# Optimization experiments

Hardware: AMD Instinct MI355X
Metric: run time of the kernel (lower is better)

## Reference

```python
import jax, jax.numpy as jnp
import numpy as np

INPUT_SIZE = 1024
HIDDEN_SIZE = 1024
LN_EPS = 1e-5


def setup_inputs() -> dict:
    key = jax.random.key(0)
    ks = jax.random.split(key, 8)
    bs, n = 4, 2048
    # Xavier-uniform bound for square (in=out) linear layers
    bound = float(np.sqrt(6.0 / (INPUT_SIZE + HIDDEN_SIZE)))
    x = jax.random.normal(ks[0], (bs, n, INPUT_SIZE), dtype=jnp.float32)
    wq = jax.random.uniform(ks[1], (INPUT_SIZE, HIDDEN_SIZE), jnp.float32, -bound, bound)
    wk = jax.random.uniform(ks[2], (INPUT_SIZE, HIDDEN_SIZE), jnp.float32, -bound, bound)
    wv = jax.random.uniform(ks[3], (INPUT_SIZE, HIDDEN_SIZE), jnp.float32, -bound, bound)
    bq = jnp.zeros((HIDDEN_SIZE,), jnp.float32)
    bk = jnp.zeros((HIDDEN_SIZE,), jnp.float32)
    bv = jnp.zeros((HIDDEN_SIZE,), jnp.float32)
    ln_w = jnp.ones((INPUT_SIZE,), jnp.float32)
    ln_b = jnp.zeros((INPUT_SIZE,), jnp.float32)
    return {"x": x, "wq": wq, "bq": bq, "wk": wk, "bk": bk,
            "wv": wv, "bv": bv, "ln_w": ln_w, "ln_b": ln_b}


def _layernorm(x, w, b):
    mu = jnp.mean(x, axis=-1, keepdims=True)
    var = jnp.mean(jnp.square(x - mu), axis=-1, keepdims=True)
    return (x - mu) * jax.lax.rsqrt(var + LN_EPS) * w + b


def reference(x, wq, bq, wk, bk, wv, bv, ln_w, ln_b):
    # x: [b, n, d_in]
    xn = _layernorm(x, ln_w, ln_b)
    q = jnp.einsum('bnd,dh->bnh', xn, wq) + bq
    k = jnp.einsum('bnd,dh->bnh', xn, wk) + bk
    v = jnp.einsum('bnd,dh->bnh', xn, wv) + bv
    scale = 1.0 / np.sqrt(HIDDEN_SIZE)
    att = jnp.einsum('bqh,bkh->bqk', q, k) * scale  # [b, n, n]
    att = jax.nn.softmax(att, axis=-1)
    out = jnp.einsum('bqk,bkh->bqh', att, v)  # [b, n, h]
    return (att, out)
```

## Files before the change

### kernel.cpp

```cpp
#include <hip/hip_runtime.h>
#include <stdint.h>


typedef __attribute__((ext_vector_type(8))) short short8;
typedef __attribute__((ext_vector_type(4))) float floatx4;
typedef __attribute__((ext_vector_type(4))) uint16_t u16x4;

__device__ __forceinline__ uint16_t f2bf(float f) {
    union { float f; uint32_t u; } v; v.f = f;
    uint32_t r = v.u + 0x7fffu + ((v.u >> 16) & 1u);
    return (uint16_t)(r >> 16);
}

typedef const uint32_t __attribute__((address_space(1)))* gas1_t;
typedef uint32_t __attribute__((address_space(3)))* las3_t;
__device__ __forceinline__ void gload_lds16(const uint16_t* g, uint16_t* l) {
    __builtin_amdgcn_global_load_lds((gas1_t)g, (las3_t)l, 16, 0, 0);
}

#define BM 128
#define BN 128
#define BK2 64

template<int EPI>
__device__ __forceinline__ void gemm_bt_body(
    const uint16_t* __restrict__ A, const uint16_t* __restrict__ Bt, int K,
    float* __restrict__ Cf, uint16_t* __restrict__ Cb, int ldc,
    const float* __restrict__ bias, float alpha)
{
    __shared__ uint16_t lA[BM * BK2];
    __shared__ uint16_t lB[BN * BK2];

    const int t  = threadIdx.x;
    const int m0 = blockIdx.y * BM;
    const int n0 = blockIdx.x * BN;

    const int srow = t >> 3;
    const int sseg = (t & 7) ^ (srow & 7);
    const uint16_t* ga = A + (size_t)(m0 + srow) * K + sseg * 8;
    const uint16_t* gb = Bt + (size_t)(n0 + srow) * K + sseg * 8;
    uint16_t* la = &lA[t * 8];
    uint16_t* lb = &lB[t * 8];
    const size_t rstep = (size_t)32 * K;

    const int lane = t & 63;
    const int w    = t >> 6;
    const int quad = lane >> 4;
    const int lrow = lane & 15;
    const int wm   = (w & 1) * 64;
    const int wn   = (w >> 1) * 64;
    const int swz  = lrow & 7;

    floatx4 acc[4][4];
#pragma unroll
    for (int i = 0; i < 4; i++)
#pragma unroll
        for (int j = 0; j < 4; j++)
            acc[i][j] = floatx4{0.f, 0.f, 0.f, 0.f};

    for (int k0 = 0; k0 < K; k0 += BK2) {
        __syncthreads();
        gload_lds16(ga + k0,             la);
        gload_lds16(ga + rstep + k0,     la + 2048);
        gload_lds16(ga + 2 * rstep + k0, la + 4096);
        gload_lds16(ga + 3 * rstep + k0, la + 6144);
        gload_lds16(gb + k0,             lb);
        gload_lds16(gb + rstep + k0,     lb + 2048);
        gload_lds16(gb + 2 * rstep + k0, lb + 4096);
        gload_lds16(gb + 3 * rstep + k0, lb + 6144);
        __syncthreads();

#pragma unroll
        for (int ks = 0; ks < 2; ks++) {
            short8 af[4], bf[4];
#pragma unroll
            for (int mi = 0; mi < 4; mi++)
                af[mi] = *(const short8*)&lA[(wm + mi * 16 + lrow) * BK2 +
                                             (((ks * 4 + quad) ^ swz) * 8)];
#pragma unroll
            for (int ni = 0; ni < 4; ni++)
                bf[ni] = *(const short8*)&lB[(wn + ni * 16 + lrow) * BK2 +
                                             (((ks * 4 + quad) ^ swz) * 8)];
#pragma unroll
            for (int mi = 0; mi < 4; mi++)
#pragma unroll
                for (int ni = 0; ni < 4; ni++)
                    acc[mi][ni] = __builtin_amdgcn_mfma_f32_16x16x32_bf16(
                        af[mi], bf[ni], acc[mi][ni], 0, 0, 0);
        }
    }

#pragma unroll
    for (int mi = 0; mi < 4; mi++) {
#pragma unroll
        for (int ni = 0; ni < 4; ni++) {
            const int row = m0 + wm + mi * 16 + quad * 4;
            const int col = n0 + wn + ni * 16 + lrow;
#pragma unroll
            for (int r = 0; r < 4; r++) {
                const float v = acc[mi][ni][r];
                if (EPI == 0) {
                    Cf[(size_t)(row + r) * ldc + col] = v * alpha;
                } else if (EPI == 1) {
                    Cb[(size_t)(row + r) * ldc + col] = f2bf(v + bias[col]);
                } else {
                    Cf[(size_t)(row + r) * ldc + col] = v;
                }
            }
        }
    }
}

__global__ __launch_bounds__(256) void k_qkv(
    const uint16_t* __restrict__ xn, const uint16_t* __restrict__ wt,
    const float* __restrict__ bq, const float* __restrict__ bk,
    const float* __restrict__ bv, uint16_t* __restrict__ qkv)
{
    const int z = blockIdx.z;
    const uint16_t* Bt = wt + (size_t)z * 1024 * 1024;
    const float* bias = (z == 0) ? bq : ((z == 1) ? bk : bv);
    uint16_t* C = qkv + (size_t)z * 8192 * 1024;
    gemm_bt_body<1>(xn, Bt, 1024, nullptr, C, 1024, bias, 0.f);
}

__global__ __launch_bounds__(256) void k_scores(
    const uint16_t* __restrict__ q, const uint16_t* __restrict__ k,
    float* __restrict__ S)
{
    const int z = blockIdx.z;
    gemm_bt_body<0>(q + (size_t)z * 2048 * 1024, k + (size_t)z * 2048 * 1024, 1024,
                    S + (size_t)z * 2048 * 2048, nullptr, 2048, nullptr, 0.03125f);
}

__global__ __launch_bounds__(256) void k_out(
    const uint16_t* __restrict__ attb, const uint16_t* __restrict__ vt,
    float* __restrict__ out)
{
    const int z = blockIdx.z;
    gemm_bt_body<2>(attb + (size_t)z * 2048 * 2048, vt + (size_t)z * 1024 * 2048, 2048,
                    out + (size_t)z * 2048 * 1024, nullptr, 1024, nullptr, 0.f);
}

__global__ __launch_bounds__(256) void k_ln(
    const float* __restrict__ x, const float* __restrict__ lw,
    const float* __restrict__ lb, uint16_t* __restrict__ xn)
{
    const int row = blockIdx.x;
    const int t = threadIdx.x;
    const float* xr = x + (size_t)row * 1024;
    const float4 xv = ((const float4*)xr)[t];
    float s  = xv.x + xv.y + xv.z + xv.w;
    float s2 = xv.x * xv.x + xv.y * xv.y + xv.z * xv.z + xv.w * xv.w;
#pragma unroll
    for (int off = 32; off > 0; off >>= 1) {
        s  += __shfl_xor(s, off);
        s2 += __shfl_xor(s2, off);
    }
    __shared__ float ps[4], ps2[4];
    const int w = t >> 6, lane = t & 63;
    if (lane == 0) { ps[w] = s; ps2[w] = s2; }
    __syncthreads();
    s  = ps[0] + ps[1] + ps[2] + ps[3];
    s2 = ps2[0] + ps2[1] + ps2[2] + ps2[3];
    const float mu  = s * (1.f / 1024.f);
    const float var = s2 * (1.f / 1024.f) - mu * mu;
    const float rs  = rsqrtf(var + 1e-5f);
    const float4 wv = ((const float4*)lw)[t];
    const float4 bv = ((const float4*)lb)[t];
    u16x4 o;
    o.x = f2bf((xv.x - mu) * rs * wv.x + bv.x);
    o.y = f2bf((xv.y - mu) * rs * wv.y + bv.y);
    o.z = f2bf((xv.z - mu) * rs * wv.z + bv.z);
    o.w = f2bf((xv.w - mu) * rs * wv.w + bv.w);
    ((u16x4*)(xn + (size_t)row * 1024))[t] = o;
}

__global__ void k_wt(const float* __restrict__ wq, const float* __restrict__ wk,
                     const float* __restrict__ wv, uint16_t* __restrict__ wt)
{
    __shared__ float tile[32][33];
    const int z = blockIdx.z;
    const float* W = (z == 0) ? wq : ((z == 1) ? wk : wv);
    uint16_t* T = wt + (size_t)z * 1024 * 1024;
    const int c0 = blockIdx.x * 32, r0 = blockIdx.y * 32;
    const int tx = threadIdx.x, ty = threadIdx.y;
#pragma unroll
    for (int i = 0; i < 4; i++)
        tile[ty + 8 * i][tx] = W[(size_t)(r0 + ty + 8 * i) * 1024 + c0 + tx];
    __syncthreads();
#pragma unroll
    for (int i = 0; i < 4; i++)
        T[(size_t)(c0 + ty + 8 * i) * 1024 + r0 + tx] = f2bf(tile[tx][ty + 8 * i]);
}

__global__ __launch_bounds__(256) void k_vt(
    const uint16_t* __restrict__ v, uint16_t* __restrict__ vt)
{
    __shared__ uint16_t tile[64][68];
    const int b = blockIdx.z;
    const uint16_t* V = v + (size_t)b * 2048 * 1024;
    uint16_t* T = vt + (size_t)b * 1024 * 2048;
    const int h0 = blockIdx.x * 64, t0 = blockIdx.y * 64;
    const int t = threadIdx.x;
    const int rr = t >> 4;
    const int cc = (t & 15) * 4;
#pragma unroll
    for (int i = 0; i < 4; i++) {
        const int tok = rr + 16 * i;
        *(u16x4*)&tile[tok][cc] =
            *(const u16x4*)&V[(size_t)(t0 + tok) * 1024 + h0 + cc];
    }
    __syncthreads();
#pragma unroll
    for (int i = 0; i < 4; i++) {
        const int h = rr + 16 * i;
        u16x4 o;
        o.x = tile[cc + 0][h];
        o.y = tile[cc + 1][h];
        o.z = tile[cc + 2][h];
        o.w = tile[cc + 3][h];
        *(u16x4*)&T[(size_t)(h0 + h) * 2048 + t0 + cc] = o;
    }
}

__global__ __launch_bounds__(256) void k_softmax(
    float* __restrict__ S, uint16_t* __restrict__ attb)
{
    const size_t row = blockIdx.x;
    float* p = S + row * 2048;
    const int t = threadIdx.x;
    float4 a = ((float4*)p)[2 * t];
    float4 b = ((float4*)p)[2 * t + 1];
    float m = fmaxf(fmaxf(fmaxf(a.x, a.y), fmaxf(a.z, a.w)),
                    fmaxf(fmaxf(b.x, b.y), fmaxf(b.z, b.w)));
#pragma unroll
    for (int off = 32; off > 0; off >>= 1) m = fmaxf(m, __shfl_xor(m, off));
    __shared__ float pm[4], pl[4];
    const int w = t >> 6, lane = t & 63;
    if (lane == 0) pm[w] = m;
    __syncthreads();
    m = fmaxf(fmaxf(pm[0], pm[1]), fmaxf(pm[2], pm[3]));

    a.x = __expf(a.x - m); a.y = __expf(a.y - m);
    a.z = __expf(a.z - m); a.w = __expf(a.w - m);
    b.x = __expf(b.x - m); b.y = __expf(b.y - m);
    b.z = __expf(b.z - m); b.w = __expf(b.w - m);
    float s = a.x + a.y + a.z + a.w + b.x + b.y + b.z + b.w;
#pragma unroll
    for (int off = 32; off > 0; off >>= 1) s += __shfl_xor(s, off);
    if (lane == 0) pl[w] = s;
    __syncthreads();
    s = pl[0] + pl[1] + pl[2] + pl[3];
    const float inv = 1.f / s;

    a.x *= inv; a.y *= inv; a.z *= inv; a.w *= inv;
    b.x *= inv; b.y *= inv; b.z *= inv; b.w *= inv;
    ((float4*)p)[2 * t]     = a;
    ((float4*)p)[2 * t + 1] = b;

    uint16_t* q = attb + row * 2048 + t * 8;
    u16x4 o0, o1;
    o0.x = f2bf(a.x); o0.y = f2bf(a.y); o0.z = f2bf(a.z); o0.w = f2bf(a.w);
    o1.x = f2bf(b.x); o1.y = f2bf(b.y); o1.z = f2bf(b.z); o1.w = f2bf(b.w);
    ((u16x4*)q)[0] = o0;
    ((u16x4*)q)[1] = o1;
}

extern "C" void kernel_launch(void* const* d_in, const int* in_sizes, int n_in,
                              void* d_out, int out_size, void* d_ws, size_t ws_size,
                              hipStream_t stream)
{
    const float* x  = (const float*)d_in[0];
    const float* wq = (const float*)d_in[1];
    const float* bq = (const float*)d_in[2];
    const float* wk = (const float*)d_in[3];
    const float* bk = (const float*)d_in[4];
    const float* wv = (const float*)d_in[5];
    const float* bv = (const float*)d_in[6];
    const float* lw = (const float*)d_in[7];
    const float* lb = (const float*)d_in[8];

    float* att = (float*)d_out;
    float* out = (float*)d_out + (size_t)16777216;

    uint16_t* xn = (uint16_t*)d_out;
    uint16_t* wt = (uint16_t*)d_out + (size_t)8388608;

    uint16_t* ws   = (uint16_t*)d_ws;
    uint16_t* q    = ws;
    uint16_t* k    = ws + (size_t)8388608;
    uint16_t* v    = ws + (size_t)2 * 8388608;
    uint16_t* vt   = ws;
    uint16_t* attb = ws + (size_t)8388608;
    uint16_t* qkv  = q;

    if (ws_size < (size_t)50331648) return;

    k_ln<<<8192, 256, 0, stream>>>(x, lw, lb, xn);
    k_wt<<<dim3(32, 32, 3), dim3(32, 8), 0, stream>>>(wq, wk, wv, wt);
    k_qkv<<<dim3(8, 64, 3), 256, 0, stream>>>(xn, wt, bq, bk, bv, qkv);
    k_scores<<<dim3(16, 16, 4), 256, 0, stream>>>(q, k, att);
    k_vt<<<dim3(16, 32, 4), 256, 0, stream>>>(v, vt);
    k_softmax<<<8192, 256, 0, stream>>>(att, attb);
    k_out<<<dim3(8, 16, 4), 256, 0, stream>>>(attb, vt, out);
}
```

Baseline: 338.0 us.

## Double-buffer LDS tiles in bf16 GEMM with K-step prefetch

Cuts the GEMM K-tile from 64 to 32 and splits LDS into two buffers. The next tile's global-to-LDS loads are issued before the current tile's MFMA work, which leaves one barrier per iteration instead of two. The aim is to overlap memory latency with compute. In exchange each barrier covers half as much MFMA work, and the XOR swizzle shrinks to 4 segments, which may raise LDS bank conflicts.

```diff
diff --git a/kernel.cpp b/kernel.cpp
--- a/kernel.cpp
+++ b/kernel.cpp
@@ -20,7 +20,7 @@
 
 #define BM 128
 #define BN 128
-#define BK2 64
+#define BKD 32
 
 template<int EPI>
 __device__ __forceinline__ void gemm_bt_body(
@@ -28,20 +28,20 @@
     float* __restrict__ Cf, uint16_t* __restrict__ Cb, int ldc,
     const float* __restrict__ bias, float alpha)
 {
-    __shared__ uint16_t lA[BM * BK2];
-    __shared__ uint16_t lB[BN * BK2];
+    __shared__ uint16_t lA[2 * BM * BKD];
+    __shared__ uint16_t lB[2 * BN * BKD];
 
     const int t  = threadIdx.x;
     const int m0 = blockIdx.y * BM;
     const int n0 = blockIdx.x * BN;
 
-    const int srow = t >> 3;
-    const int sseg = (t & 7) ^ (srow & 7);
+    const int srow = t >> 2;
+    const int sseg = (t & 3) ^ (srow & 3);
     const uint16_t* ga = A + (size_t)(m0 + srow) * K + sseg * 8;
     const uint16_t* gb = Bt + (size_t)(n0 + srow) * K + sseg * 8;
-    uint16_t* la = &lA[t * 8];
-    uint16_t* lb = &lB[t * 8];
-    const size_t rstep = (size_t)32 * K;
+    const size_t row64 = (size_t)64 * K;
+    uint16_t* laslot0[2] = { &lA[t * 8], &lA[4096 + t * 8] };
+    uint16_t* lbslot0[2] = { &lB[t * 8], &lB[4096 + t * 8] };
 
     const int lane = t & 63;
     const int w    = t >> 6;
@@ -49,7 +49,7 @@
     const int lrow = lane & 15;
     const int wm   = (w & 1) * 64;
     const int wn   = (w >> 1) * 64;
-    const int swz  = lrow & 7;
+    const int pseg = (quad ^ (lrow & 3)) * 8;
 
     floatx4 acc[4][4];
 #pragma unroll
@@ -58,36 +58,37 @@
         for (int j = 0; j < 4; j++)
             acc[i][j] = floatx4{0.f, 0.f, 0.f, 0.f};
 
-    for (int k0 = 0; k0 < K; k0 += BK2) {
+    gload_lds16(ga,         laslot0[0]);
+    gload_lds16(ga + row64, laslot0[0] + 2048);
+    gload_lds16(gb,         lbslot0[0]);
+    gload_lds16(gb + row64, lbslot0[0] + 2048);
+
+    int cur = 0;
+    for (int k0 = 0; k0 < K; k0 += BKD) {
         __syncthreads();
-        gload_lds16(ga + k0,             la);
-        gload_lds16(ga + rstep + k0,     la + 2048);
-        gload_lds16(ga + 2 * rstep + k0, la + 4096);
-        gload_lds16(ga + 3 * rstep + k0, la + 6144);
-        gload_lds16(gb + k0,             lb);
-        gload_lds16(gb + rstep + k0,     lb + 2048);
-        gload_lds16(gb + 2 * rstep + k0, lb + 4096);
-        gload_lds16(gb + 3 * rstep + k0, lb + 6144);
-        __syncthreads();
-
-#pragma unroll
-        for (int ks = 0; ks < 2; ks++) {
-            short8 af[4], bf[4];
-#pragma unroll
-            for (int mi = 0; mi < 4; mi++)
-                af[mi] = *(const short8*)&lA[(wm + mi * 16 + lrow) * BK2 +
-                                             (((ks * 4 + quad) ^ swz) * 8)];
+        if (k0 + BKD < K) {
+            const int nxt = cur ^ 1;
+            gload_lds16(ga + (k0 + BKD),         laslot0[nxt]);
+            gload_lds16(ga + row64 + (k0 + BKD), laslot0[nxt] + 2048);
+            gload_lds16(gb + (k0 + BKD),         lbslot0[nxt]);
+            gload_lds16(gb + row64 + (k0 + BKD), lbslot0[nxt] + 2048);
+        }
+        const uint16_t* bufA = &lA[cur * 4096];
+        const uint16_t* bufB = &lB[cur * 4096];
+        short8 af[4], bf[4];
+#pragma unroll
+        for (int mi = 0; mi < 4; mi++)
+            af[mi] = *(const short8*)&bufA[(wm + mi * 16 + lrow) * BKD + pseg];
+#pragma unroll
+        for (int ni = 0; ni < 4; ni++)
+            bf[ni] = *(const short8*)&bufB[(wn + ni * 16 + lrow) * BKD + pseg];
+#pragma unroll
+        for (int mi = 0; mi < 4; mi++)
 #pragma unroll
             for (int ni = 0; ni < 4; ni++)
-                bf[ni] = *(const short8*)&lB[(wn + ni * 16 + lrow) * BK2 +
-                                             (((ks * 4 + quad) ^ swz) * 8)];
-#pragma unroll
-            for (int mi = 0; mi < 4; mi++)
-#pragma unroll
-                for (int ni = 0; ni < 4; ni++)
-                    acc[mi][ni] = __builtin_amdgcn_mfma_f32_16x16x32_bf16(
-                        af[mi], bf[ni], acc[mi][ni], 0, 0, 0);
-        }
+                acc[mi][ni] = __builtin_amdgcn_mfma_f32_16x16x32_bf16(
+                    af[mi], bf[ni], acc[mi][ni], 0, 0, 0);
+        cur ^= 1;
     }
 
 #pragma unroll
```

Result: slower. 350.1 us (+3.6%).
